# Kernel optimization log

Measured on AMD Instinct MI355X. Metric: run time of the kernel, lower is better.

The kernel has to match this reference:

```python
import jax, jax.numpy as jnp
import numpy as np

T = 65536
OBS_DIM = 64
ACTION_DIM = 16
EMB_DIM = 8  # min(action_dim, 8)
HID = 256
NOBJ = 4
IN_DIM = OBS_DIM + EMB_DIM


def setup_inputs() -> dict:
    key = jax.random.key(0)
    ks = jax.random.split(key, 16)
    g = lambda k, shape, s=0.05: (jax.random.normal(k, shape, dtype=jnp.float32) * s)
    inp = {
        "observations": jax.random.normal(ks[0], (T, OBS_DIM), dtype=jnp.float32),
        "actions": jax.random.randint(ks[1], (T,), 0, ACTION_DIM),
        "emb": g(ks[2], (ACTION_DIM, EMB_DIM)),
        # layer 0 (input_dim -> hidden)
        "Win0": g(ks[3], (HID, IN_DIM)),
        "WB0": g(ks[4], (HID, IN_DIM)),
        "WC0": g(ks[5], (HID, IN_DIM)),
        "Wd0": g(ks[6], (HID, IN_DIM)),
        "Alog0": jax.random.normal(ks[7], (HID,), dtype=jnp.float32),
        # layer 1 (hidden -> hidden)
        "Win1": g(ks[8], (HID, HID)),
        "WB1": g(ks[9], (HID, HID)),
        "WC1": g(ks[10], (HID, HID)),
        "Wd1": g(ks[11], (HID, HID)),
        "Alog1": jax.random.normal(ks[12], (HID,), dtype=jnp.float32),
        # output head
        "Wout": g(ks[13], (NOBJ, HID)),
        "bout": jnp.zeros((NOBJ,), dtype=jnp.float32),
    }
    return inp


def _ssm_layer(x, Win, WB, WC, Wd, Alog):
    """One selective-SSM layer: h_t = exp(delta_t * A) * h_{t-1} + B_t * x_state_t; y = C * h."""
    x_state = x @ Win.T            # [T, H]
    B = x @ WB.T                   # [T, H]
    C = x @ WC.T                   # [T, H]
    delta = jax.nn.sigmoid(x @ Wd.T)  # [T, H]
    A = -jnp.exp(Alog)             # [H]
    A_bar = jnp.exp(delta * A)     # [T, H], decay factors
    Bx = B * x_state               # [T, H], inputs to the recurrence

    def step(h, inputs):
        a, bx = inputs
        h = a * h + bx
        return h, h

    h0 = jnp.zeros((x_state.shape[-1],), dtype=x_state.dtype)
    _, h_seq = jax.lax.scan(step, h0, (A_bar, Bx))
    return C * h_seq


def reference(observations, actions, emb,
              Win0, WB0, WC0, Wd0, Alog0,
              Win1, WB1, WC1, Wd1, Alog1,
              Wout, bout):
    x = jnp.concatenate([observations, emb[actions]], axis=-1)  # [T, IN_DIM]
    x = _ssm_layer(x, Win0, WB0, WC0, Wd0, Alog0)
    x = _ssm_layer(x, Win1, WB1, WC1, Wd1, Alog1)
    out = x @ Wout.T + bout                                     # [T, NOBJ]
    return jax.nn.softplus(out) + 1.0
```

## Files before the change

### kernel.cpp

```cpp
#include <hip/hip_runtime.h>

typedef unsigned short u16;
typedef __attribute__((ext_vector_type(8))) short bf16x8;
typedef __attribute__((ext_vector_type(4))) float f32x4;
typedef __attribute__((ext_vector_type(8))) unsigned short u16x8;

#define T_LEN 65536
#define HID 256
#define K0 96
#define K1 256
#define BM 128
#define BN 128
#define CHUNK 64
#define NCHUNK 1024
#define NSEG 32
#define CPS 32

__device__ __forceinline__ float bf2f(u16 u) {
  unsigned x = ((unsigned)u) << 16; float f; __builtin_memcpy(&f, &x, 4); return f;
}
__device__ __forceinline__ u16 f2bf(float f) {
  unsigned x; __builtin_memcpy(&x, &f, 4);
  x += 0x7FFFu + ((x >> 16) & 1u);
  return (u16)(x >> 16);
}

__device__ __forceinline__ void gl_lds16(const void* g, void* l) {
  __builtin_amdgcn_global_load_lds((const __attribute__((address_space(1))) unsigned int*)g,
                                   (__attribute__((address_space(3))) unsigned int*)l,
                                   16, 0, 0);
}

__global__ __launch_bounds__(256) void build_x0(
    const float* __restrict__ obs, const int* __restrict__ act,
    const float* __restrict__ emb, u16* __restrict__ x0)
{
  const int idx = blockIdx.x * 256 + threadIdx.x;
  const int t = idx / 24, seg = idx - t * 24;
  u16 v0 = 0, v1 = 0, v2 = 0, v3 = 0;
  if (seg < 16) {
    const float4 f = *(const float4*)&obs[(size_t)t * 64 + seg * 4];
    v0 = f2bf(f.x); v1 = f2bf(f.y); v2 = f2bf(f.z); v3 = f2bf(f.w);
  } else if (seg < 18) {
    const int a = act[t];
    const int e0 = (seg - 16) * 4;
    v0 = f2bf(emb[a * 8 + e0 + 0]); v1 = f2bf(emb[a * 8 + e0 + 1]);
    v2 = f2bf(emb[a * 8 + e0 + 2]); v3 = f2bf(emb[a * 8 + e0 + 3]);
  }
  u16* p = &x0[(size_t)t * 96 + seg * 4];
  p[0] = v0; p[1] = v1; p[2] = v2; p[3] = v3;
}

__global__ __launch_bounds__(256) void prep_w(
    const float* __restrict__ Win0, const float* __restrict__ WB0,
    const float* __restrict__ WC0,  const float* __restrict__ Wd0,
    const float* __restrict__ Alog0,
    const float* __restrict__ Win1, const float* __restrict__ WB1,
    const float* __restrict__ WC1,  const float* __restrict__ Wd1,
    const float* __restrict__ Alog1,
    u16* __restrict__ W0v, u16* __restrict__ W1v, float* __restrict__ Aneg)
{
  const int idx = blockIdx.x * 256 + threadIdx.x;
  if (idx < 1024 * K0) {
    const int row = idx / K0, k = idx - row * K0;
    const int h = row >> 2, p = row & 3;
    const float* W = (p == 0) ? Win0 : (p == 1) ? WB0 : (p == 2) ? WC0 : Wd0;
    W0v[idx] = f2bf((k < 72) ? W[h * 72 + k] : 0.f);
  } else if (idx < 1024 * K0 + 1024 * K1) {
    const int j = idx - 1024 * K0;
    const int row = j >> 8, k = j & 255;
    const int h = row >> 2, p = row & 3;
    const float* W = (p == 0) ? Win1 : (p == 1) ? WB1 : (p == 2) ? WC1 : Wd1;
    W1v[j] = f2bf(W[h * 256 + k]);
  } else if (idx < 1024 * K0 + 1024 * K1 + 512) {
    const int j = idx - (1024 * K0 + 1024 * K1);
    Aneg[j] = -__expf((j < 256) ? Alog0[j] : Alog1[j - 256]);
  }
}

template <int KDIM>
__global__ __launch_bounds__(256, 4) void gemm_scan(
    const u16* __restrict__ X, const u16* __restrict__ Wv,
    const float* __restrict__ Aneg,
    unsigned* __restrict__ uvb,
    float* __restrict__ aprod, float* __restrict__ hlast)
{
  static_assert(KDIM % 32 == 0, "K must be multiple of 32");
  constexpr int NK = KDIM / 32;
  __shared__ alignas(16) char smem[33792];
  __shared__ float sAgg[8 * 32 * 2];
  float* sT = (float*)smem;

  const int tid = threadIdx.x;
  const int l   = tid & 63;
  const int w   = tid >> 6;
  const int bid = blockIdx.x;
  const int xcd = bid & 7;
  const int k_  = bid >> 3;
  const int mt  = xcd * 64 + (k_ >> 3);
  const int nt  = k_ & 7;
  const int m0  = mt * BM;
  const int n0  = nt * BN;
  const int wm  = (w >> 1) * 64;
  const int wn  = (w & 1) * 64;

  f32x4 acc[4][4];
  const f32x4 zero = {0.f, 0.f, 0.f, 0.f};
#pragma unroll
  for (int mi = 0; mi < 4; ++mi)
#pragma unroll
    for (int ni = 0; ni < 4; ++ni) acc[mi][ni] = zero;

  const int rr = w * 32 + (l >> 2);
  const int kb = (l & 3) * 16;

#define STAGE(KS, BUF)                                                          \
  {                                                                             \
    _Pragma("unroll")                                                           \
    for (int i = 0; i < 2; ++i) {                                               \
      const char* gA = (const char*)(X + (size_t)(m0 + rr + i * 16) * KDIM + (KS) * 32) + kb; \
      gl_lds16(gA, smem + (BUF) * 16384 + w * 2048 + i * 1024);                 \
      const char* gB = (const char*)(Wv + (size_t)(n0 + rr + i * 16) * KDIM + (KS) * 32) + kb; \
      gl_lds16(gB, smem + (BUF) * 16384 + 8192 + w * 2048 + i * 1024);          \
    }                                                                           \
  }

  STAGE(0, 0);
  int cur = 0;
  for (int ks = 0; ks < NK; ++ks) {
    if (ks + 1 < NK) {
      STAGE(ks + 1, cur ^ 1);
      asm volatile("s_waitcnt vmcnt(4)" ::: "memory");
    } else {
      asm volatile("s_waitcnt vmcnt(0)" ::: "memory");
    }
    __builtin_amdgcn_s_barrier();
    asm volatile("" ::: "memory");

    const u16* sA = (const u16*)(smem + cur * 16384);
    const u16* sB = (const u16*)(smem + cur * 16384 + 8192);
    bf16x8 af[4], bfr[4];
#pragma unroll
    for (int mi = 0; mi < 4; ++mi)
      af[mi] = *(const bf16x8*)&sA[(wm + mi * 16 + (l & 15)) * 32 + (l >> 4) * 8];
#pragma unroll
    for (int ni = 0; ni < 4; ++ni)
      bfr[ni] = *(const bf16x8*)&sB[(wn + ni * 16 + (l & 15)) * 32 + (l >> 4) * 8];
#pragma unroll
    for (int mi = 0; mi < 4; ++mi)
#pragma unroll
      for (int ni = 0; ni < 4; ++ni)
        acc[mi][ni] = __builtin_amdgcn_mfma_f32_16x16x32_bf16(af[mi], bfr[ni], acc[mi][ni], 0, 0, 0);

    asm volatile("s_waitcnt lgkmcnt(0)" ::: "memory");
    __builtin_amdgcn_s_barrier();
    asm volatile("" ::: "memory");
    cur ^= 1;
  }

  const int q  = tid >> 5;
  const int c  = tid & 31;
  const int ch = (n0 >> 2) + c;
  const float An = Aneg[ch];

  for (int hh = 0; hh < 2; ++hh) {
    __syncthreads();
    if ((w >> 1) == hh) {
#pragma unroll
      for (int mi = 0; mi < 4; ++mi)
#pragma unroll
        for (int ni = 0; ni < 4; ++ni)
#pragma unroll
          for (int v = 0; v < 4; ++v)
            sT[(mi * 16 + (l >> 4) * 4 + v) * 132 + wn + ni * 16 + (l & 15)] = acc[mi][ni][v];
    }
    __syncthreads();

    float Pl[8], Hl[8], Cl[8];
    float ap = 1.f, hl = 0.f;
#pragma unroll
    for (int j = 0; j < 8; ++j) {
      const int tl = q * 8 + j;
      const f32x4 pv = *(const f32x4*)&sT[tl * 132 + 4 * c];
      const float delta = 1.f / (1.f + __expf(-pv[3]));
      const float a  = __expf(delta * An);
      hl = a * hl + pv[1] * pv[0];
      ap *= a;
      Pl[j] = ap; Hl[j] = hl; Cl[j] = pv[2];
    }
    sAgg[(q * 32 + c) * 2 + 0] = ap;
    sAgg[(q * 32 + c) * 2 + 1] = hl;
    __syncthreads();

    float sap = 1.f, shl = 0.f;
    for (int qq = 0; qq < q; ++qq) {
      const float a_ = sAgg[(qq * 32 + c) * 2 + 0];
      const float h_ = sAgg[(qq * 32 + c) * 2 + 1];
      shl = a_ * shl + h_;
      sap *= a_;
    }
#pragma unroll
    for (int j = 0; j < 8; ++j) {
      const int tl = q * 8 + j;
      const float hloc = Hl[j] + Pl[j] * shl;
      const float vpfx = Pl[j] * sap;
      const unsigned pack = (unsigned)f2bf(Cl[j] * hloc)
                          | ((unsigned)f2bf(Cl[j] * vpfx) << 16);
      uvb[(size_t)(m0 + hh * 64 + tl) * HID + ch] = pack;
    }
    if (q == 7) {
      const int chunk = mt * 2 + hh;
      aprod[(size_t)chunk * HID + ch] = sap * ap;
      hlast[(size_t)chunk * HID + ch] = Hl[7] + Pl[7] * shl;
    }
  }
#undef STAGE
}

__global__ __launch_bounds__(256) void pass2a(
    const float* __restrict__ aprod, const float* __restrict__ hlast,
    float* __restrict__ clocal, float* __restrict__ apfxc,
    float* __restrict__ segAP, float* __restrict__ segHL)
{
  const int s = blockIdx.x;
  const int h = threadIdx.x;
  float H = 0.f, P = 1.f;
#pragma unroll 4
  for (int j = 0; j < CPS; ++j) {
    const size_t o = (size_t)(s * CPS + j) * HID + h;
    clocal[o] = H; apfxc[o] = P;
    const float a = aprod[o], hh = hlast[o];
    H = a * H + hh;
    P *= a;
  }
  segAP[s * HID + h] = P;
  segHL[s * HID + h] = H;
}

__global__ __launch_bounds__(256) void pass2b(
    const float* __restrict__ segAP, const float* __restrict__ segHL,
    float* __restrict__ segc)
{
  const int h = threadIdx.x;
  float S = 0.f;
#pragma unroll 4
  for (int s = 0; s < NSEG; ++s) {
    segc[s * HID + h] = S;
    S = segAP[s * HID + h] * S + segHL[s * HID + h];
  }
}

__global__ __launch_bounds__(256) void combine(
    const unsigned* __restrict__ uvb,
    const float* __restrict__ clocal, const float* __restrict__ apfxc,
    const float* __restrict__ segc, u16* __restrict__ y)
{
  const size_t vi = (size_t)blockIdx.x * 256 + threadIdx.x;
  const int t   = (int)(vi >> 5);
  const int ch0 = ((int)vi & 31) * 8;
  const int ck  = t >> 6;
  const int sg  = ck / CPS;
  const float* cl = &clocal[(size_t)ck * HID + ch0];
  const float* ax = &apfxc[(size_t)ck * HID + ch0];
  const float* sc = &segc[(size_t)sg * HID + ch0];
  const float4 cl0 = *(const float4*)&cl[0], cl1 = *(const float4*)&cl[4];
  const float4 ax0 = *(const float4*)&ax[0], ax1 = *(const float4*)&ax[4];
  const float4 sc0 = *(const float4*)&sc[0], sc1 = *(const float4*)&sc[4];
  const float crv[8] = {
    cl0.x + ax0.x * sc0.x, cl0.y + ax0.y * sc0.y,
    cl0.z + ax0.z * sc0.z, cl0.w + ax0.w * sc0.w,
    cl1.x + ax1.x * sc1.x, cl1.y + ax1.y * sc1.y,
    cl1.z + ax1.z * sc1.z, cl1.w + ax1.w * sc1.w };
  const uint4 p0 = *(const uint4*)&uvb[vi * 8];
  const uint4 p1 = *(const uint4*)&uvb[vi * 8 + 4];
  const unsigned pk[8] = {p0.x, p0.y, p0.z, p0.w, p1.x, p1.y, p1.z, p1.w};
  u16x8 o;
#pragma unroll
  for (int j = 0; j < 8; ++j)
    o[j] = f2bf(bf2f((u16)(pk[j] & 0xffffu)) + bf2f((u16)(pk[j] >> 16)) * crv[j]);
  *(u16x8*)&y[vi * 8] = o;
}

__global__ __launch_bounds__(256) void head(
    const u16* __restrict__ y1, const float* __restrict__ Wout,
    const float* __restrict__ bout, float* __restrict__ out)
{
  __shared__ u16 ly[64 * 264];
  __shared__ float lw[4 * HID];
  __shared__ float lb[4];
  const int tid = threadIdx.x;
  for (int i = tid; i < 4 * HID; i += 256) lw[i] = Wout[i];
  if (tid < 4) lb[tid] = bout[tid];
  const size_t rbase = (size_t)blockIdx.x * 64 * HID;
#pragma unroll
  for (int i = 0; i < 8; ++i) {
    const int lin = i * 256 + tid;
    const int r = lin >> 5, c8 = lin & 31;
    *(u16x8*)&ly[r * 264 + c8 * 8] = *(const u16x8*)&y1[rbase + (size_t)r * HID + c8 * 8];
  }
  __syncthreads();
  const int t = tid >> 2, o = tid & 3;
  float acc = lb[o];
#pragma unroll 8
  for (int h = 0; h < HID; ++h)
    acc += bf2f(ly[t * 264 + h]) * lw[o * HID + h];
  out[((size_t)blockIdx.x * 64 + t) * 4 + o] = logf(1.f + __expf(acc)) + 1.f;
}

extern "C" void kernel_launch(void* const* d_in, const int* in_sizes, int n_in,
                              void* d_out, int out_size, void* d_ws, size_t ws_size,
                              hipStream_t stream)
{
  (void)in_sizes; (void)n_in; (void)out_size; (void)ws_size;
  const float* obs   = (const float*)d_in[0];
  const int*   act   = (const int*)d_in[1];
  const float* emb   = (const float*)d_in[2];
  const float* Win0  = (const float*)d_in[3];
  const float* WB0   = (const float*)d_in[4];
  const float* WC0   = (const float*)d_in[5];
  const float* Wd0   = (const float*)d_in[6];
  const float* Alog0 = (const float*)d_in[7];
  const float* Win1  = (const float*)d_in[8];
  const float* WB1   = (const float*)d_in[9];
  const float* WC1   = (const float*)d_in[10];
  const float* Wd1   = (const float*)d_in[11];
  const float* Alog1 = (const float*)d_in[12];
  const float* Wout  = (const float*)d_in[13];
  const float* bout  = (const float*)d_in[14];
  float* out = (float*)d_out;

  char* ws = (char*)d_ws;
  size_t off = 0;
  auto alloc = [&](size_t bytes) {
    char* p = ws + off;
    off += (bytes + 255) & ~(size_t)255;
    return p;
  };
  u16*      x0    = (u16*)     alloc((size_t)T_LEN * K0 * 2);
  u16*      W0v   = (u16*)     alloc((size_t)1024 * K0 * 2);
  u16*      W1v   = (u16*)     alloc((size_t)1024 * K1 * 2);
  float*    Aneg  = (float*)   alloc(512 * 4);
  unsigned* uvb   = (unsigned*)alloc((size_t)T_LEN * HID * 4);
  u16*      y     = (u16*)     alloc((size_t)T_LEN * HID * 2);
  float*    aprod = (float*)   alloc((size_t)NCHUNK * HID * 4);
  float*    hlast = (float*)   alloc((size_t)NCHUNK * HID * 4);
  float*    clocal= (float*)   alloc((size_t)NCHUNK * HID * 4);
  float*    apfxc = (float*)   alloc((size_t)NCHUNK * HID * 4);
  float*    segAP = (float*)   alloc((size_t)NSEG * HID * 4);
  float*    segHL = (float*)   alloc((size_t)NSEG * HID * 4);
  float*    segc  = (float*)   alloc((size_t)NSEG * HID * 4);

  build_x0<<<T_LEN * 24 / 256, 256, 0, stream>>>(obs, act, emb, x0);
  prep_w<<<(1024 * K0 + 1024 * K1 + 512 + 255) / 256, 256, 0, stream>>>(
      Win0, WB0, WC0, Wd0, Alog0, Win1, WB1, WC1, Wd1, Alog1, W0v, W1v, Aneg);

  gemm_scan<K0><<<4096, 256, 0, stream>>>(x0, W0v, Aneg, uvb, aprod, hlast);
  pass2a<<<NSEG, 256, 0, stream>>>(aprod, hlast, clocal, apfxc, segAP, segHL);
  pass2b<<<1, 256, 0, stream>>>(segAP, segHL, segc);
  combine<<<T_LEN * HID / 8 / 256, 256, 0, stream>>>(uvb, clocal, apfxc, segc, y);

  gemm_scan<K1><<<4096, 256, 0, stream>>>(y, W1v, Aneg + 256, uvb, aprod, hlast);
  pass2a<<<NSEG, 256, 0, stream>>>(aprod, hlast, clocal, apfxc, segAP, segHL);
  pass2b<<<1, 256, 0, stream>>>(segAP, segHL, segc);
  combine<<<T_LEN * HID / 8 / 256, 256, 0, stream>>>(uvb, clocal, apfxc, segc, y);

  head<<<T_LEN / 64, 256, 0, stream>>>(y, Wout, bout, out);
}
```

Baseline: 274.8 us.

## Permute weight rows so each wave scans in registers with shuffles instead of LDS

The fused weight matrices are reordered so that within each 64-column wave tile, the four 16-column MFMA subtiles hold the in, B, C and delta projections for the same 16 channels. Each lane can then run the chunk scan directly on its accumulator registers, with a cross-lane shuffle prefix that combines the 4-row groups inside each 16-row tile. This removes the LDS transpose of the accumulator tile, the scan aggregate buffer and several block barriers. In exchange there are more shuffles and a longer serial dependency chain per lane, and the uvb stores now come from a different lane mapping, which may coalesce differently.

```diff
diff --git a/kernel.cpp b/kernel.cpp
--- a/kernel.cpp
+++ b/kernel.cpp
@@ -63,13 +63,15 @@
   const int idx = blockIdx.x * 256 + threadIdx.x;
   if (idx < 1024 * K0) {
     const int row = idx / K0, k = idx - row * K0;
-    const int h = row >> 2, p = row & 3;
+    const int p = (row >> 4) & 3;
+    const int h = (row >> 6) * 16 + (row & 15);
     const float* W = (p == 0) ? Win0 : (p == 1) ? WB0 : (p == 2) ? WC0 : Wd0;
     W0v[idx] = f2bf((k < 72) ? W[h * 72 + k] : 0.f);
   } else if (idx < 1024 * K0 + 1024 * K1) {
     const int j = idx - 1024 * K0;
     const int row = j >> 8, k = j & 255;
-    const int h = row >> 2, p = row & 3;
+    const int p = (row >> 4) & 3;
+    const int h = (row >> 6) * 16 + (row & 15);
     const float* W = (p == 0) ? Win1 : (p == 1) ? WB1 : (p == 2) ? WC1 : Wd1;
     W1v[j] = f2bf(W[h * 256 + k]);
   } else if (idx < 1024 * K0 + 1024 * K1 + 512) {
@@ -87,9 +89,7 @@
 {
   static_assert(KDIM % 32 == 0, "K must be multiple of 32");
   constexpr int NK = KDIM / 32;
-  __shared__ alignas(16) char smem[33792];
-  __shared__ float sAgg[8 * 32 * 2];
-  float* sT = (float*)smem;
+  __shared__ alignas(16) char smem[32768];
 
   const int tid = threadIdx.x;
   const int l   = tid & 63;
@@ -157,64 +157,68 @@
     asm volatile("" ::: "memory");
     cur ^= 1;
   }
-
-  const int q  = tid >> 5;
-  const int c  = tid & 31;
-  const int ch = (n0 >> 2) + c;
+#undef STAGE
+
+  const int lg = l >> 4;
+  const int cc = l & 15;
+  const int ch = (n0 >> 2) + (wn >> 6) * 16 + cc;
+  const int chunk = mt * 2 + (wm >> 6);
   const float An = Aneg[ch];
 
-  for (int hh = 0; hh < 2; ++hh) {
-    __syncthreads();
-    if ((w >> 1) == hh) {
-#pragma unroll
-      for (int mi = 0; mi < 4; ++mi)
-#pragma unroll
-        for (int ni = 0; ni < 4; ++ni)
-#pragma unroll
-          for (int v = 0; v < 4; ++v)
-            sT[(mi * 16 + (l >> 4) * 4 + v) * 132 + wn + ni * 16 + (l & 15)] = acc[mi][ni][v];
+  float Pl[4][4], Hl[4][4], Cv[4][4];
+  float P3[4], H3[4];
+#pragma unroll
+  for (int mi = 0; mi < 4; ++mi) {
+    float ap = 1.f, hl = 0.f;
+#pragma unroll
+    for (int v = 0; v < 4; ++v) {
+      const float pin = acc[mi][0][v];
+      const float pB  = acc[mi][1][v];
+      const float pC  = acc[mi][2][v];
+      const float pd  = acc[mi][3][v];
+      const float delta = 1.f / (1.f + __expf(-pd));
+      const float a  = __expf(delta * An);
+      hl = a * hl + pB * pin;
+      ap *= a;
+      Pl[mi][v] = ap; Hl[mi][v] = hl; Cv[mi][v] = pC;
     }
-    __syncthreads();
-
-    float Pl[8], Hl[8], Cl[8];
-    float ap = 1.f, hl = 0.f;
-#pragma unroll
-    for (int j = 0; j < 8; ++j) {
-      const int tl = q * 8 + j;
-      const f32x4 pv = *(const f32x4*)&sT[tl * 132 + 4 * c];
-      const float delta = 1.f / (1.f + __expf(-pv[3]));
-      const float a  = __expf(delta * An);
-      hl = a * hl + pv[1] * pv[0];
-      ap *= a;
-      Pl[j] = ap; Hl[j] = hl; Cl[j] = pv[2];
+    P3[mi] = ap; H3[mi] = hl;
+  }
+
+  float aL[4], hL[4], aT[4], hT[4];
+#pragma unroll
+  for (int mi = 0; mi < 4; ++mi) {
+    float al = 1.f, hlx = 0.f, at = 1.f, ht = 0.f;
+#pragma unroll
+    for (int s = 0; s < 4; ++s) {
+      const float Ab = __shfl(P3[mi], cc + s * 16, 64);
+      const float Hb = __shfl(H3[mi], cc + s * 16, 64);
+      if (s < lg) { hlx = Ab * hlx + Hb; al *= Ab; }
+      ht = Ab * ht + Hb; at *= Ab;
     }
-    sAgg[(q * 32 + c) * 2 + 0] = ap;
-    sAgg[(q * 32 + c) * 2 + 1] = hl;
-    __syncthreads();
-
-    float sap = 1.f, shl = 0.f;
-    for (int qq = 0; qq < q; ++qq) {
-      const float a_ = sAgg[(qq * 32 + c) * 2 + 0];
-      const float h_ = sAgg[(qq * 32 + c) * 2 + 1];
-      shl = a_ * shl + h_;
-      sap *= a_;
+    aL[mi] = al; hL[mi] = hlx; aT[mi] = at; hT[mi] = ht;
+  }
+
+  float aM = 1.f, hM = 0.f;
+#pragma unroll
+  for (int mi = 0; mi < 4; ++mi) {
+    const float a_pre = aL[mi] * aM;
+    const float h_pre = aL[mi] * hM + hL[mi];
+#pragma unroll
+    for (int v = 0; v < 4; ++v) {
+      const float Pt = Pl[mi][v] * a_pre;
+      const float Ht = Pl[mi][v] * h_pre + Hl[mi][v];
+      const unsigned pack = (unsigned)f2bf(Cv[mi][v] * Ht)
+                          | ((unsigned)f2bf(Cv[mi][v] * Pt) << 16);
+      uvb[(size_t)(m0 + wm + mi * 16 + lg * 4 + v) * HID + ch] = pack;
     }
-#pragma unroll
-    for (int j = 0; j < 8; ++j) {
-      const int tl = q * 8 + j;
-      const float hloc = Hl[j] + Pl[j] * shl;
-      const float vpfx = Pl[j] * sap;
-      const unsigned pack = (unsigned)f2bf(Cl[j] * hloc)
-                          | ((unsigned)f2bf(Cl[j] * vpfx) << 16);
-      uvb[(size_t)(m0 + hh * 64 + tl) * HID + ch] = pack;
-    }
-    if (q == 7) {
-      const int chunk = mt * 2 + hh;
-      aprod[(size_t)chunk * HID + ch] = sap * ap;
-      hlast[(size_t)chunk * HID + ch] = Hl[7] + Pl[7] * shl;
-    }
-  }
-#undef STAGE
+    hM = aT[mi] * hM + hT[mi];
+    aM *= aT[mi];
+  }
+  if (lg == 0) {
+    aprod[(size_t)chunk * HID + ch] = aM;
+    hlast[(size_t)chunk * HID + ch] = hM;
+  }
 }
 
 __global__ __launch_bounds__(256) void pass2a(
```

New measurement: 263.1 us. 1.04x faster.
